# Performance work log

Measured on AMD Instinct MI355X. Metric: run time of the kernel, lower is better.

Reference implementation:

```python
import jax, jax.numpy as jnp
import numpy as np

HEAD_SIZE = 64


def setup_inputs() -> dict:
    key = jax.random.key(0)
    kx, kq, kk, kv = jax.random.split(key, 4)
    B, L, D = 4, 4096, 1024
    scale = 1.0 / np.sqrt(D)
    x = jax.random.normal(kx, (B, L, D), dtype=jnp.float32)
    Wq = jax.random.normal(kq, (D, HEAD_SIZE), dtype=jnp.float32) * scale
    Wk = jax.random.normal(kk, (D, HEAD_SIZE), dtype=jnp.float32) * scale
    Wv = jax.random.normal(kv, (D, HEAD_SIZE), dtype=jnp.float32) * scale
    return {"x": x, "Wq": Wq, "Wk": Wk, "Wv": Wv}


def reference(x, Wq, Wk, Wv):
    B, L, D = x.shape
    H = Wq.shape[1]
    q = jnp.einsum('bld,dh->blh', x, Wq)  # [B,L,H]
    k = jnp.einsum('bld,dh->blh', x, Wk)
    v = jnp.einsum('bld,dh->blh', x, Wv)
    # full L x L score matrix, as in the original module
    scores = jnp.einsum('bqh,bkh->bqk', q, k) / jnp.sqrt(jnp.float32(H))
    causal = jnp.tril(jnp.ones((L, L), dtype=bool))
    scores = jnp.where(causal, scores, -jnp.inf)
    attn = jax.nn.softmax(scores, axis=-1)
    z = jnp.einsum('bqk,bkh->bqh', attn, v)  # [B,L,H]
    return z
```

## Files before the change

### kernel.cpp

```cpp
#include <hip/hip_runtime.h>
#include <stdint.h>

#define L_SEQ 4096
#define D_MODEL 1024
#define HEAD 64
#define KCH 512
#define MAXCH 8
#define NQT 32

typedef unsigned short u16;
typedef _Float16 f16;
typedef __attribute__((ext_vector_type(8))) f16 f16x8;
typedef __attribute__((ext_vector_type(2))) __fp16 fp16x2;
typedef __attribute__((ext_vector_type(4))) float f32x4;

static __device__ __forceinline__ u16 f16bits(float f) {
    union { f16 h; u16 u; } c; c.h = (f16)f; return c.u;
}
static __device__ __forceinline__ uint32_t pk16(float a, float b) {
    union { fp16x2 h; uint32_t u; } c;
    c.h = __builtin_amdgcn_cvt_pkrtz(a, b);
    return c.u;
}
static __device__ __forceinline__ f16x8 ld8h(const u16* p) { return *(const f16x8*)p; }

static __device__ __forceinline__ f32x4 mfma16h(f16x8 a, f16x8 b, f32x4 c) {
    return __builtin_amdgcn_mfma_f32_16x16x32_f16(a, b, c, 0, 0, 0);
}

static __device__ __forceinline__ void gload16(const u16* g, u16* l) {
    __builtin_amdgcn_global_load_lds(
        (const __attribute__((address_space(1))) void*)g,
        (__attribute__((address_space(3))) void*)l, 16, 0, 0);
}

static __device__ __forceinline__ int Sq(int qt) {
    int f = qt >> 2, r = qt & 3;
    return (f + 1) * (2 * f + r);
}

__global__ __launch_bounds__(256) void conv_w(
    const float* __restrict__ Wq, const float* __restrict__ Wk,
    const float* __restrict__ Wv, u16* __restrict__ Wt)
{
    __shared__ u16 tile[64][72];
    const float* W = (blockIdx.y == 0) ? Wq : (blockIdx.y == 1) ? Wk : Wv;
    const float sc = (blockIdx.y == 0) ? 0.18033688f : 1.0f;
    u16* dst = Wt + blockIdx.y * (HEAD * D_MODEL);
    const int k0 = blockIdx.x * 64, t = threadIdx.x;
    #pragma unroll
    for (int i = 0; i < 16; i++) {
        int idx = i * 256 + t;
        int kk = idx >> 6, h = idx & 63;
        tile[h][kk] = f16bits(W[(size_t)(k0 + kk) * HEAD + h] * sc);
    }
    __syncthreads();
    #pragma unroll
    for (int i = 0; i < 16; i++) {
        int idx = i * 256 + t;
        int h = idx >> 6, kk = idx & 63;
        dst[(size_t)h * D_MODEL + k0 + kk] = tile[h][kk];
    }
}

__global__ __launch_bounds__(512, 4) void qkv_proj(
    const float* __restrict__ x, const u16* __restrict__ Wt,
    u16* __restrict__ qb, u16* __restrict__ kb, u16* __restrict__ vTb)
{
    __shared__ __align__(16) u16 Wl[2 * 192 * 32];
    __shared__ __align__(16) u16 Xl[2 * 32 * 36];
#define WLX(dh,r,c) Wl[((dh)*192 + (r))*32 + (c)]
#define XLX(kh,r,c) Xl[((kh)*32  + (r))*36 + (c)]
#define CT(r,c)     Wl[(r)*200 + (c)]

    const int t = threadIdx.x;
    const int wv = t >> 6, lane = t & 63;
    const int ln16 = lane & 15, quad = lane >> 4;
    const int mt = wv >> 2;
    const int j0 = (wv & 3) * 3;
    const int m0 = blockIdx.x * 32;

    f32x4 acc[3] = {};
    float4 xv;

    auto issueW = [&](int s) {
        const int k0 = s * 64;
        #pragma unroll
        for (int i = 0; i < 3; i++) {
            int c = i * 8 + wv;
            int dh = c / 12, rw = (c % 12) * 16 + (lane >> 2), col = (lane & 3) * 8;
            gload16(Wt + (size_t)rw * D_MODEL + k0 + dh * 32 + col,
                    &WLX(dh, rw, col));
        }
    };
    auto loadx = [&](int s) {
        xv = *(const float4*)&x[(size_t)(m0 + (t >> 4)) * D_MODEL + s * 64 + (t & 15) * 4];
    };
    auto packx = [&]() {
        int cs = (t & 15) * 4;
        uint2 p; p.x = pk16(xv.x, xv.y); p.y = pk16(xv.z, xv.w);
        *(uint2*)&XLX(cs >> 5, t >> 4, cs & 31) = p;
    };

    loadx(0); issueW(0); packx();
    for (int s = 0; s < 16; s++) {
        __syncthreads();
        f16x8 xb[2], af[2][3];
        #pragma unroll
        for (int c = 0; c < 2; c++) {
            xb[c] = ld8h(&XLX(c, mt * 16 + ln16, quad * 8));
            #pragma unroll
            for (int j = 0; j < 3; j++)
                af[c][j] = ld8h(&WLX(c, (j0 + j) * 16 + ln16, quad * 8));
        }
        #pragma unroll
        for (int c = 0; c < 2; c++)
            #pragma unroll
            for (int j = 0; j < 3; j++)
                acc[j] = mfma16h(af[c][j], xb[c], acc[j]);
        if (s + 1 < 16) loadx(s + 1);
        __syncthreads();
        if (s + 1 < 16) { issueW(s + 1); packx(); }
    }

    __syncthreads();
    #pragma unroll
    for (int j = 0; j < 3; j++) {
        int g0 = (j0 + j) * 16 + quad * 4;
        uint2 pk;
        pk.x = pk16(acc[j][0], acc[j][1]);
        pk.y = pk16(acc[j][2], acc[j][3]);
        *(uint2*)&CT(mt * 16 + ln16, g0) = pk;
    }
    __syncthreads();
    {
        int tt = t & 255, mrow = tt >> 3, hseg = (tt & 7) * 8;
        if (t < 256)
            *(f16x8*)&qb[(size_t)(m0 + mrow) * HEAD + hseg] = *(f16x8*)&CT(mrow, hseg);
        else
            *(f16x8*)&kb[(size_t)(m0 + mrow) * HEAD + hseg] = *(f16x8*)&CT(mrow, 64 + hseg);
        if (t < 256) {
            int h = t >> 2, mloc = (t & 3) * 8;
            f16x8 vvv;
            #pragma unroll
            for (int jj = 0; jj < 8; jj++)
                ((u16*)&vvv)[jj] = CT(mloc + jj, 128 + h);
            int bbt = m0 >> 12, l0 = m0 & 4095;
            *(f16x8*)&vTb[(size_t)(bbt * HEAD + h) * L_SEQ + l0 + mloc] = vvv;
        }
    }
#undef WLX
#undef XLX
#undef CT
}

__global__ __launch_bounds__(256, 4) void attn_chunk(
    const u16* __restrict__ qb, const u16* __restrict__ kb,
    const u16* __restrict__ vT, u16* __restrict__ OpartH,
    float* __restrict__ lpart, float* __restrict__ out)
{
    const int qt = blockIdx.x, ch = blockIdx.y, b = blockIdx.z;
    if (ch * KCH > qt * 128 + 127) return;

    __shared__ __align__(16) u16 Kls[2 * 64 * 32];
    __shared__ __align__(16) u16 Vls[2 * 64 * 32];
    __shared__ __align__(16) u16 Pls[4 * 32 * 72];
#define KBX(dh,r,c) Kls[((dh)*64 + (r))*32 + (c)]
#define VBX(kh,r,c) Vls[((kh)*64 + (r))*32 + (c)]
#define PX(r,c)     Pls[((wv)*32 + (r))*72 + (c)]

    const int t = threadIdx.x, wv = t >> 6, lane = t & 63;
    const int ln16 = lane & 15, quad = lane >> 4;
    const int qmin = qt * 128 + wv * 32;
    const int nch = (qt + 4) >> 2;

    f16x8 qf[2][2];
    #pragma unroll
    for (int qn = 0; qn < 2; qn++) {
        const u16* qrp = qb + (size_t)(b * L_SEQ + qmin + qn * 16 + ln16) * HEAD + quad * 8;
        qf[qn][0] = ld8h(qrp); qf[qn][1] = ld8h(qrp + 32);
    }

    const u16* kbb = kb + (size_t)b * L_SEQ * HEAD;
    const u16* vbb = vT + (size_t)b * HEAD * L_SEQ;

    f32x4 o[2][4] = {};
    float lsum[2] = {0.f, 0.f};

    const int kv_lo = ch * KCH;
    const int kv_hi = min(kv_lo + KCH, qt * 128 + 128);
    const int nst = (kv_hi - kv_lo) >> 6;

    auto issue_stage = [&](int kv0) {
        #pragma unroll
        for (int k2 = 0; k2 < 4; k2++) {
            int c = wv * 4 + k2;
            if (c < 8) {
                int dh = c & 1, g = c >> 1;
                const u16* gp = kbb + (size_t)(kv0 + g * 16 + (lane >> 2)) * HEAD
                                    + dh * 32 + (lane & 3) * 8;
                gload16(gp, &KBX(dh, g * 16 + (lane >> 2), (lane & 3) * 8));
            } else {
                int c2 = c - 8, kh = c2 & 1, g = c2 >> 1;
                const u16* gp = vbb + (size_t)(g * 16 + (lane >> 2)) * L_SEQ
                                    + kv0 + kh * 32 + (lane & 3) * 8;
                gload16(gp, &VBX(kh, g * 16 + (lane >> 2), (lane & 3) * 8));
            }
        }
    };

    for (int s = 0; s < nst; s++) {
        const int kv0 = kv_lo + s * 64;
        issue_stage(kv0);
        __syncthreads();

        #pragma unroll
        for (int g = 0; g < 4; g++) {
            f16x8 ka0 = ld8h(&KBX(0, g * 16 + ln16, quad * 8));
            f16x8 ka1 = ld8h(&KBX(1, g * 16 + ln16, quad * 8));
            #pragma unroll
            for (int qn = 0; qn < 2; qn++) {
                f32x4 s2 = {};
                s2 = mfma16h(ka0, qf[qn][0], s2);
                s2 = mfma16h(ka1, qf[qn][1], s2);
                float p0, p1, p2, p3;
                if (kv0 + g * 16 + 15 <= qmin + qn * 16) {
                    p0 = __builtin_amdgcn_exp2f(s2[0]);
                    p1 = __builtin_amdgcn_exp2f(s2[1]);
                    p2 = __builtin_amdgcn_exp2f(s2[2]);
                    p3 = __builtin_amdgcn_exp2f(s2[3]);
                } else {
                    int q = qmin + qn * 16 + ln16;
                    int kv = kv0 + g * 16 + quad * 4;
                    p0 = (kv     <= q) ? __builtin_amdgcn_exp2f(s2[0]) : 0.f;
                    p1 = (kv + 1 <= q) ? __builtin_amdgcn_exp2f(s2[1]) : 0.f;
                    p2 = (kv + 2 <= q) ? __builtin_amdgcn_exp2f(s2[2]) : 0.f;
                    p3 = (kv + 3 <= q) ? __builtin_amdgcn_exp2f(s2[3]) : 0.f;
                }
                lsum[qn] += (p0 + p1) + (p2 + p3);
                uint2 pk; pk.x = pk16(p0, p1); pk.y = pk16(p2, p3);
                *(uint2*)&PX(qn * 16 + ln16, g * 16 + quad * 4) = pk;
            }
        }
        f16x8 pf[2][2];
        #pragma unroll
        for (int qn = 0; qn < 2; qn++) {
            pf[qn][0] = ld8h(&PX(qn * 16 + ln16, quad * 8));
            pf[qn][1] = ld8h(&PX(qn * 16 + ln16, 32 + quad * 8));
        }
        #pragma unroll
        for (int hg = 0; hg < 4; hg++) {
            f16x8 va0 = ld8h(&VBX(0, hg * 16 + ln16, quad * 8));
            f16x8 va1 = ld8h(&VBX(1, hg * 16 + ln16, quad * 8));
            #pragma unroll
            for (int qn = 0; qn < 2; qn++) {
                o[qn][hg] = mfma16h(va0, pf[qn][0], o[qn][hg]);
                o[qn][hg] = mfma16h(va1, pf[qn][1], o[qn][hg]);
            }
        }
        __syncthreads();
    }

    #pragma unroll
    for (int qn = 0; qn < 2; qn++) {
        lsum[qn] += __shfl_xor(lsum[qn], 16);
        lsum[qn] += __shfl_xor(lsum[qn], 32);
    }

    if (nch == 1) {
        #pragma unroll
        for (int qn = 0; qn < 2; qn++) {
            float inv = 1.f / lsum[qn];
            int qg = qmin + qn * 16 + ln16;
            #pragma unroll
            for (int hg = 0; hg < 4; hg++) {
                f32x4 r = o[qn][hg];
                float4 w; w.x = r[0] * inv; w.y = r[1] * inv; w.z = r[2] * inv; w.w = r[3] * inv;
                *(float4*)&out[((size_t)(b * L_SEQ + qg)) * HEAD + hg * 16 + quad * 4] = w;
            }
        }
        return;
    }

    const size_t base = (size_t)(b * 144 + Sq(qt) + ch);
    #pragma unroll
    for (int qn = 0; qn < 2; qn++) {
        int q_local = wv * 32 + qn * 16 + ln16;
        #pragma unroll
        for (int hg = 0; hg < 4; hg++) {
            uint2 pk;
            pk.x = pk16(o[qn][hg][0], o[qn][hg][1]);
            pk.y = pk16(o[qn][hg][2], o[qn][hg][3]);
            *(uint2*)&OpartH[base * 8192 + (size_t)q_local * 64 + hg * 16 + quad * 4] = pk;
        }
        if (quad == 0)
            lpart[base * 128 + q_local] = lsum[qn];
    }
#undef KBX
#undef VBX
#undef PX
}

__global__ __launch_bounds__(256) void merge_chunks(
    const u16* __restrict__ OpartH, const float* __restrict__ lpart,
    float* __restrict__ out)
{
    const int qt = blockIdx.x + 4, qseg = blockIdx.y, b = blockIdx.z;
    const int nch = (qt + 4) >> 2;
    const int t = threadIdx.x;
    const int slot0 = b * 144 + Sq(qt);
    #pragma unroll
    for (int i = 0; i < 2; i++) {
        int idx = i * 256 + t;
        int q = qseg * 32 + (idx >> 4), hgp = idx & 15;
        float L = 0.f, a0 = 0.f, a1 = 0.f, a2 = 0.f, a3 = 0.f;
        for (int c = 0; c < nch; c++) {
            L += lpart[(size_t)(slot0 + c) * 128 + q];
            union { uint2 u; f16 h[4]; } v;
            v.u = *(const uint2*)&OpartH[(size_t)(slot0 + c) * 8192 + q * 64 + hgp * 4];
            a0 += (float)v.h[0]; a1 += (float)v.h[1];
            a2 += (float)v.h[2]; a3 += (float)v.h[3];
        }
        float inv = 1.f / L;
        float4 r; r.x = a0 * inv; r.y = a1 * inv; r.z = a2 * inv; r.w = a3 * inv;
        *(float4*)&out[((size_t)(b * L_SEQ + qt * 128 + q)) * HEAD + hgp * 4] = r;
    }
}

extern "C" void kernel_launch(void* const* d_in, const int* in_sizes, int n_in,
                              void* d_out, int out_size, void* d_ws, size_t ws_size,
                              hipStream_t stream) {
    const float* x  = (const float*)d_in[0];
    const float* Wq = (const float*)d_in[1];
    const float* Wk = (const float*)d_in[2];
    const float* Wv = (const float*)d_in[3];
    float* out = (float*)d_out;

    u16* ws16 = (u16*)d_ws;
    u16* Wt  = ws16;
    u16* qb  = Wt + 3 * HEAD * D_MODEL;
    u16* kb  = qb + 16384 * HEAD;
    u16* vTb = kb + 16384 * HEAD;
    u16* OpartH = vTb + 16384 * HEAD;
    float* lpart = (float*)(OpartH + (size_t)4 * 144 * 8192);

    conv_w      <<<dim3(16, 3), 256, 0, stream>>>(Wq, Wk, Wv, Wt);
    qkv_proj    <<<dim3(512), 512, 0, stream>>>(x, Wt, qb, kb, vTb);
    attn_chunk  <<<dim3(NQT, MAXCH, 4), 256, 0, stream>>>(qb, kb, vTb, OpartH, lpart, out);
    merge_chunks<<<dim3(28, 4, 4), 256, 0, stream>>>(OpartH, lpart, out);
}
```

Baseline: 153.1 us.

## Double-buffer K tiles in LDS and load V directly into registers

K tiles are now double-buffered in shared memory. The next tile's load is issued right after the loop-top barrier, so it overlaps the current tile's compute, and the trailing barrier is removed. V is no longer staged through LDS: each wave loads its V fragments straight from global memory into registers. This removes one barrier per iteration and lets K loads overlap compute, but every wave now fetches the full V tile redundantly through the cache hierarchy. The single-barrier scheme is only correct if the asynchronous K loads have completed before the barrier.

After: 188.4 us. 23.0% more time.

```diff
diff --git a/kernel.cpp b/kernel.cpp
--- a/kernel.cpp
+++ b/kernel.cpp
@@ -162,12 +162,10 @@
     const int qt = blockIdx.x, ch = blockIdx.y, b = blockIdx.z;
     if (ch * KCH > qt * 128 + 127) return;
 
-    __shared__ __align__(16) u16 Kls[2 * 64 * 32];
-    __shared__ __align__(16) u16 Vls[2 * 64 * 32];
+    __shared__ __align__(16) u16 Kls[2 * 2 * 64 * 32];
     __shared__ __align__(16) u16 Pls[4 * 32 * 72];
-#define KBX(dh,r,c) Kls[((dh)*64 + (r))*32 + (c)]
-#define VBX(kh,r,c) Vls[((kh)*64 + (r))*32 + (c)]
-#define PX(r,c)     Pls[((wv)*32 + (r))*72 + (c)]
+#define KBX(bb,dh,r,c) Kls[(((bb)*2 + (dh))*64 + (r))*32 + (c)]
+#define PX(r,c)        Pls[((wv)*32 + (r))*72 + (c)]
 
     const int t = threadIdx.x, wv = t >> 6, lane = t & 63;
     const int ln16 = lane & 15, quad = lane >> 4;
@@ -191,33 +189,36 @@
     const int kv_hi = min(kv_lo + KCH, qt * 128 + 128);
     const int nst = (kv_hi - kv_lo) >> 6;
 
-    auto issue_stage = [&](int kv0) {
-        #pragma unroll
-        for (int k2 = 0; k2 < 4; k2++) {
-            int c = wv * 4 + k2;
-            if (c < 8) {
-                int dh = c & 1, g = c >> 1;
-                const u16* gp = kbb + (size_t)(kv0 + g * 16 + (lane >> 2)) * HEAD
-                                    + dh * 32 + (lane & 3) * 8;
-                gload16(gp, &KBX(dh, g * 16 + (lane >> 2), (lane & 3) * 8));
-            } else {
-                int c2 = c - 8, kh = c2 & 1, g = c2 >> 1;
-                const u16* gp = vbb + (size_t)(g * 16 + (lane >> 2)) * L_SEQ
-                                    + kv0 + kh * 32 + (lane & 3) * 8;
-                gload16(gp, &VBX(kh, g * 16 + (lane >> 2), (lane & 3) * 8));
-            }
+    auto issueK = [&](int kv0, int bb) {
+        #pragma unroll
+        for (int k2 = 0; k2 < 2; k2++) {
+            int c = wv * 2 + k2;
+            int dh = c & 1, g = c >> 1;
+            const u16* gp = kbb + (size_t)(kv0 + g * 16 + (lane >> 2)) * HEAD
+                                + dh * 32 + (lane & 3) * 8;
+            gload16(gp, &KBX(bb, dh, g * 16 + (lane >> 2), (lane & 3) * 8));
         }
     };
 
+    issueK(kv_lo, 0);
+    int buf = 0;
     for (int s = 0; s < nst; s++) {
         const int kv0 = kv_lo + s * 64;
-        issue_stage(kv0);
         __syncthreads();
+        if (s + 1 < nst) issueK(kv0 + 64, buf ^ 1);
+
+        f16x8 vf[4][2];
+        #pragma unroll
+        for (int hg = 0; hg < 4; hg++) {
+            const u16* vr = vbb + (size_t)(hg * 16 + ln16) * L_SEQ + kv0 + quad * 8;
+            vf[hg][0] = ld8h(vr);
+            vf[hg][1] = ld8h(vr + 32);
+        }
 
         #pragma unroll
         for (int g = 0; g < 4; g++) {
-            f16x8 ka0 = ld8h(&KBX(0, g * 16 + ln16, quad * 8));
-            f16x8 ka1 = ld8h(&KBX(1, g * 16 + ln16, quad * 8));
+            f16x8 ka0 = ld8h(&KBX(buf, 0, g * 16 + ln16, quad * 8));
+            f16x8 ka1 = ld8h(&KBX(buf, 1, g * 16 + ln16, quad * 8));
             #pragma unroll
             for (int qn = 0; qn < 2; qn++) {
                 f32x4 s2 = {};
@@ -250,15 +251,13 @@
         }
         #pragma unroll
         for (int hg = 0; hg < 4; hg++) {
-            f16x8 va0 = ld8h(&VBX(0, hg * 16 + ln16, quad * 8));
-            f16x8 va1 = ld8h(&VBX(1, hg * 16 + ln16, quad * 8));
             #pragma unroll
             for (int qn = 0; qn < 2; qn++) {
-                o[qn][hg] = mfma16h(va0, pf[qn][0], o[qn][hg]);
-                o[qn][hg] = mfma16h(va1, pf[qn][1], o[qn][hg]);
+                o[qn][hg] = mfma16h(vf[hg][0], pf[qn][0], o[qn][hg]);
+                o[qn][hg] = mfma16h(vf[hg][1], pf[qn][1], o[qn][hg]);
             }
         }
-        __syncthreads();
+        buf ^= 1;
     }
 
     #pragma unroll
@@ -297,7 +296,6 @@
             lpart[base * 128 + q_local] = lsum[qn];
     }
 #undef KBX
-#undef VBX
 #undef PX
 }
 
```
